# Performance work log

Measured on AMD Instinct MI355X. Metric: run time of the kernel, lower is better.

Reference implementation:

```python
import jax, jax.numpy as jnp
import numpy as np

D = 32        # number of TT cores (d)
R = 16        # tt_rank
B = 262144    # batch size


def setup_inputs() -> dict:
    key = jax.random.key(0)
    k1, k2, k3, k4 = jax.random.split(key, 4)
    return {
        "X": jax.random.randint(k1, (B, D), 0, 2, dtype=jnp.int32),
        "core_first": jax.random.normal(k2, (1, R, 2), dtype=jnp.float32),
        "cores_mid": jax.random.normal(k3, (D - 2, R, R, 2), dtype=jnp.float32),
        "core_last": jax.random.normal(k4, (R, 1, 2), dtype=jnp.float32),
    }


def reference(X, core_first, cores_mid, core_last):
    # First core: cores[0][:, :, X[:,0]] -> [1, R, B] -> permute -> [B, 1, R].
    # We carry the squeezed [B, R] row vector instead of [B, 1, R].
    carry0 = jnp.take(core_first[0], X[:, 0], axis=-1).T  # [B, R]

    def step(carry, inp):
        core, idx = inp                       # core: [R, R, 2], idx: [B]
        c = jnp.take(core, idx, axis=2)       # gathered core: [R, R, B]
        new = jnp.einsum('br,rsb->bs', carry, c)  # batched (1xR)@(RxR)
        return new, None

    # Middle cores i = 1 .. D-2 (sequential chain, data-dependent).
    carry, _ = jax.lax.scan(step, carry0, (cores_mid, X[:, 1:D - 1].T))

    # Last core: cores[-1][:, :, X[:,-1]] -> [R, 1, B]; contract to scalar per batch.
    c_last = jnp.take(core_last[:, 0, :], X[:, -1], axis=-1)  # [R, B]
    out = jnp.einsum('br,rb->b', carry, c_last)               # [B]  (squeeze of [B,1,1])
    return out
```

## Files before the change

kernel.cpp:

```cpp
#include <hip/hip_runtime.h>


#define R 16
#define TT_D 32
#define BATCH 262144

#define OFF_V4   0
#define OFF_A    256
#define OFF_B    (256 + 1*4096)
#define OFF_C    (256 + 2*4096)
#define OFF_Dm   (256 + 3*4096)
#define OFF_E    (256 + 4*4096)
#define OFF_F    (256 + 5*4096)
#define OFF_W4   (256 + 6*4096)
#define OFF_V8   (OFF_W4 + 256)
#define OFF_P8   (OFF_V8 + 4096)
#define OFF_Q8   (OFF_P8 + 65536)
#define OFF_W8   (OFF_Q8 + 65536)
#define OFF_V16  (OFF_W8 + 4096)
#define OFF_W16  (OFF_V16 + 1048576)
#define WS_FLOATS (OFF_W16 + 1048576)

__global__ __launch_bounds__(256) void tt_nibble(const float* __restrict__ cf,
                                                 const float* __restrict__ cm,
                                                 const float* __restrict__ cl,
                                                 float* __restrict__ ws) {
    const int tbl = blockIdx.x;
    const int t = threadIdx.x;

    if (tbl >= 1 && tbl <= 6) {
        const int e = t >> 4, r = t & 15;
        const int base = 3 + (tbl - 1) * 4;
        const int b0 = (e >> 3) & 1, b1 = (e >> 2) & 1, b2 = (e >> 1) & 1, b3 = e & 1;
        float v[R], nv[R];
        const float* M0 = cm + base * 512;
        #pragma unroll
        for (int s2 = 0; s2 < R; s2++) v[s2] = M0[(r * 16 + s2) * 2 + b0];
        const int bits[3] = { b1, b2, b3 };
        for (int k = 1; k <= 3; k++) {
            const float* M = cm + (base + k) * 512;
            const int bb = bits[k - 1];
            #pragma unroll
            for (int s2 = 0; s2 < R; s2++) {
                float acc = 0.f;
                #pragma unroll
                for (int tt = 0; tt < R; tt++) acc += v[tt] * M[(tt * 16 + s2) * 2 + bb];
                nv[s2] = acc;
            }
            #pragma unroll
            for (int s2 = 0; s2 < R; s2++) v[s2] = nv[s2];
        }
        float* o = ws + OFF_A + (tbl - 1) * 4096 + e * 256 + r * 16;
        #pragma unroll
        for (int s2 = 0; s2 < R; s2++) o[s2] = v[s2];
    } else if (tbl == 0) {
        if (t < 16) {
            const int e = t;
            const int b0 = (e >> 3) & 1, b1 = (e >> 2) & 1, b2 = (e >> 1) & 1, b3 = e & 1;
            float v[R], nv[R];
            #pragma unroll
            for (int s2 = 0; s2 < R; s2++) v[s2] = cf[s2 * 2 + b0];
            const int bits[3] = { b1, b2, b3 };
            for (int k = 1; k <= 3; k++) {
                const float* M = cm + (k - 1) * 512;
                const int bb = bits[k - 1];
                #pragma unroll
                for (int s2 = 0; s2 < R; s2++) {
                    float acc = 0.f;
                    #pragma unroll
                    for (int tt = 0; tt < R; tt++) acc += v[tt] * M[(tt * 16 + s2) * 2 + bb];
                    nv[s2] = acc;
                }
                #pragma unroll
                for (int s2 = 0; s2 < R; s2++) v[s2] = nv[s2];
            }
            float* o = ws + OFF_V4 + e * 16;
            #pragma unroll
            for (int s2 = 0; s2 < R; s2++) o[s2] = v[s2];
        }
    } else {
        if (t < 16) {
            const int e = t;
            const int b0 = (e >> 3) & 1, b1 = (e >> 2) & 1, b2 = (e >> 1) & 1, b3 = e & 1;
            float w[R], nw[R];
            #pragma unroll
            for (int r2 = 0; r2 < R; r2++) w[r2] = cl[r2 * 2 + b3];
            const int cores[3] = { 29, 28, 27 };
            const int bits[3] = { b2, b1, b0 };
            for (int k = 0; k < 3; k++) {
                const float* M = cm + cores[k] * 512;
                const int bb = bits[k];
                #pragma unroll
                for (int r2 = 0; r2 < R; r2++) {
                    float acc = 0.f;
                    #pragma unroll
                    for (int tt = 0; tt < R; tt++) acc += M[(r2 * 16 + tt) * 2 + bb] * w[tt];
                    nw[r2] = acc;
                }
                #pragma unroll
                for (int r2 = 0; r2 < R; r2++) w[r2] = nw[r2];
            }
            float* o = ws + OFF_W4 + e * 16;
            #pragma unroll
            for (int r2 = 0; r2 < R; r2++) o[r2] = w[r2];
        }
    }
}

__global__ __launch_bounds__(256) void tt_byte(float* __restrict__ ws) {
    const int g = blockIdx.x;
    const int t = threadIdx.x;
    if (g < 32) {
        const bool isP = (g < 16);
        const int idx = (isP ? g : g - 16) * 256 + t;
        const int e = idx >> 4, r = idx & 15;
        const int h = e >> 4, l = e & 15;
        const float* Hm = ws + (isP ? OFF_B : OFF_Dm) + h * 256;
        const float* Lm = ws + (isP ? OFF_C : OFF_E) + l * 256;
        float hrow[R];
        #pragma unroll
        for (int k = 0; k < R; k++) hrow[k] = Hm[r * 16 + k];
        float outv[R];
        #pragma unroll
        for (int s2 = 0; s2 < R; s2++) outv[s2] = 0.f;
        #pragma unroll
        for (int k = 0; k < R; k++) {
            const float a = hrow[k];
            #pragma unroll
            for (int s2 = 0; s2 < R; s2++) outv[s2] += a * Lm[k * 16 + s2];
        }
        float* o = ws + (isP ? OFF_P8 : OFF_Q8) + e * 256 + r * 16;
        #pragma unroll
        for (int s2 = 0; s2 < R; s2++) o[s2] = outv[s2];
    } else if (g == 32) {
        const int e = t, h = e >> 4, l = e & 15;
        const float* v4 = ws + OFF_V4 + h * 16;
        const float* Am = ws + OFF_A + l * 256;
        float outv[R];
        #pragma unroll
        for (int s2 = 0; s2 < R; s2++) outv[s2] = 0.f;
        #pragma unroll
        for (int k = 0; k < R; k++) {
            const float a = v4[k];
            #pragma unroll
            for (int s2 = 0; s2 < R; s2++) outv[s2] += a * Am[k * 16 + s2];
        }
        float* o = ws + OFF_V8 + e * 16;
        #pragma unroll
        for (int s2 = 0; s2 < R; s2++) o[s2] = outv[s2];
    } else {
        const int e = t, h = e >> 4, l = e & 15;
        const float* Fm = ws + OFF_F + h * 256;
        const float* w4 = ws + OFF_W4 + l * 16;
        float outv[R];
        #pragma unroll
        for (int r2 = 0; r2 < R; r2++) {
            float acc = 0.f;
            #pragma unroll
            for (int k = 0; k < R; k++) acc += Fm[r2 * 16 + k] * w4[k];
            outv[r2] = acc;
        }
        float* o = ws + OFF_W8 + e * 16;
        #pragma unroll
        for (int r2 = 0; r2 < R; r2++) o[r2] = outv[r2];
    }
}

__global__ __launch_bounds__(256) void tt_final(float* __restrict__ ws) {
    const int t = threadIdx.x;
    if (blockIdx.x < 256) {
        const int h = blockIdx.x, l = t;
        __shared__ float sv[16];
        if (t < 16) sv[t] = ws[OFF_V8 + h * 16 + t];
        __syncthreads();
        const float* P = ws + OFF_P8 + l * 256;
        float outv[R];
        #pragma unroll
        for (int s2 = 0; s2 < R; s2++) outv[s2] = 0.f;
        #pragma unroll
        for (int r2 = 0; r2 < R; r2++) {
            const float a = sv[r2];
            #pragma unroll
            for (int s2 = 0; s2 < R; s2++) outv[s2] += a * P[r2 * 16 + s2];
        }
        float* o = ws + OFF_V16 + (size_t)(h * 256 + l) * 16;
        #pragma unroll
        for (int s2 = 0; s2 < R; s2++) o[s2] = outv[s2];
    } else {
        const int h = blockIdx.x - 256, l = t;
        __shared__ float sQ[256];
        sQ[t] = ws[OFF_Q8 + h * 256 + t];
        __syncthreads();
        const float* wv = ws + OFF_W8 + l * 16;
        float w[R];
        #pragma unroll
        for (int k = 0; k < R; k++) w[k] = wv[k];
        float outv[R];
        #pragma unroll
        for (int r2 = 0; r2 < R; r2++) {
            float acc = 0.f;
            #pragma unroll
            for (int k = 0; k < R; k++) acc += sQ[r2 * 16 + k] * w[k];
            outv[r2] = acc;
        }
        float* o = ws + OFF_W16 + (size_t)(h * 256 + l) * 16;
        #pragma unroll
        for (int r2 = 0; r2 < R; r2++) o[r2] = outv[r2];
    }
}

__global__ __launch_bounds__(256) void tt_main(const int* __restrict__ X,
                                               const float* __restrict__ ws,
                                               float* __restrict__ out) {
    const int b = blockIdx.x * 256 + threadIdx.x;
    const int4* Xr = (const int4*)(X + (size_t)b * TT_D);
    int xv[TT_D];
    #pragma unroll
    for (int q = 0; q < 8; q++) {
        int4 c = Xr[q];
        xv[q * 4 + 0] = c.x; xv[q * 4 + 1] = c.y; xv[q * 4 + 2] = c.z; xv[q * 4 + 3] = c.w;
    }
    unsigned p = 0, s = 0;
    #pragma unroll
    for (int i = 0; i < 16; i++) p = (p << 1) | (unsigned)(xv[i] & 1);
    #pragma unroll
    for (int i = 16; i < 32; i++) s = (s << 1) | (unsigned)(xv[i] & 1);

    const float4* v = (const float4*)(ws + OFF_V16 + (size_t)p * 16);
    const float4* w = (const float4*)(ws + OFF_W16 + (size_t)s * 16);
    float acc = 0.f;
    #pragma unroll
    for (int k = 0; k < 4; k++) {
        float4 a = v[k], c = w[k];
        acc += a.x * c.x + a.y * c.y + a.z * c.z + a.w * c.w;
    }
    out[b] = acc;
}

__global__ __launch_bounds__(256) void tt_direct(const int* __restrict__ X,
                                                 const float* __restrict__ cf,
                                                 const float* __restrict__ cm,
                                                 const float* __restrict__ cl,
                                                 float* __restrict__ out) {
    __shared__ float scm[30 * 16 * 16 * 2];
    for (int i = threadIdx.x; i < 30 * 16 * 16 * 2; i += blockDim.x) scm[i] = cm[i];
    __syncthreads();
    const int b = blockIdx.x * blockDim.x + threadIdx.x;
    if (b >= BATCH) return;
    const int* xr = X + (size_t)b * TT_D;
    float v[R], nv[R];
    const int x0 = xr[0] & 1;
    #pragma unroll
    for (int r = 0; r < R; r++) v[r] = cf[r * 2 + x0];
    for (int i = 1; i <= 30; i++) {
        const int bit = xr[i] & 1;
        const float* M = scm + (i - 1) * 512;
        #pragma unroll
        for (int s2 = 0; s2 < R; s2++) {
            float acc = 0.f;
            #pragma unroll
            for (int r = 0; r < R; r++) acc += v[r] * M[(r * 16 + s2) * 2 + bit];
            nv[s2] = acc;
        }
        #pragma unroll
        for (int s2 = 0; s2 < R; s2++) v[s2] = nv[s2];
    }
    const int xl = xr[31] & 1;
    float acc = 0.f;
    #pragma unroll
    for (int r = 0; r < R; r++) acc += v[r] * cl[r * 2 + xl];
    out[b] = acc;
}

extern "C" void kernel_launch(void* const* d_in, const int* in_sizes, int n_in,
                              void* d_out, int out_size, void* d_ws, size_t ws_size,
                              hipStream_t stream) {
    const int* X = (const int*)d_in[0];
    const float* cf = (const float*)d_in[1];
    const float* cm = (const float*)d_in[2];
    const float* cl = (const float*)d_in[3];
    float* out = (float*)d_out;

    if (ws_size >= (size_t)WS_FLOATS * sizeof(float)) {
        float* ws = (float*)d_ws;
        tt_nibble<<<8, 256, 0, stream>>>(cf, cm, cl, ws);
        tt_byte<<<34, 256, 0, stream>>>(ws);
        tt_final<<<512, 256, 0, stream>>>(ws);
        tt_main<<<BATCH / 256, 256, 0, stream>>>(X, ws, out);
    } else {
        tt_direct<<<(BATCH + 255) / 256, 256, 0, stream>>>(X, cf, cm, cl, out);
    }
}
```

Before: 122.8 us.

## Merge nibble and byte table builds into one kernel; process two rows per thread

Folds the nibble-level and byte-level table construction into one kernel that stages the cores in shared memory with a transposed layout, which cuts one launch and the global round trip for the intermediate tables. The main lookup kernel now handles two batch rows per thread, using nontemporal vector loads of X and a packed float2 nontemporal store. This reduces launch overhead and aims for better memory-level parallelism, at the cost of higher register use and less parallelism inside the build kernel.

```diff
diff --git a/kernel.cpp b/kernel.cpp
--- a/kernel.cpp
+++ b/kernel.cpp
@@ -5,15 +5,7 @@
 #define TT_D 32
 #define BATCH 262144
 
-#define OFF_V4   0
-#define OFF_A    256
-#define OFF_B    (256 + 1*4096)
-#define OFF_C    (256 + 2*4096)
-#define OFF_Dm   (256 + 3*4096)
-#define OFF_E    (256 + 4*4096)
-#define OFF_F    (256 + 5*4096)
-#define OFF_W4   (256 + 6*4096)
-#define OFF_V8   (OFF_W4 + 256)
+#define OFF_V8   0
 #define OFF_P8   (OFF_V8 + 4096)
 #define OFF_Q8   (OFF_P8 + 65536)
 #define OFF_W8   (OFF_Q8 + 65536)
@@ -21,220 +13,272 @@
 #define OFF_W16  (OFF_V16 + 1048576)
 #define WS_FLOATS (OFF_W16 + 1048576)
 
-__global__ __launch_bounds__(256) void tt_nibble(const float* __restrict__ cf,
+typedef int   v4i __attribute__((ext_vector_type(4)));
+typedef float v4f __attribute__((ext_vector_type(4)));
+typedef float v2f __attribute__((ext_vector_type(2)));
+
+__device__ inline void row_chain4(const float* __restrict__ Lc, int cbase, int e, int r,
+                                  float* __restrict__ v) {
+    const int b0 = (e >> 3) & 1, b1 = (e >> 2) & 1, b2 = (e >> 1) & 1, b3 = e & 1;
+    #pragma unroll
+    for (int s = 0; s < 16; s++) v[s] = Lc[((((cbase * 2 + b0) * 16) + s) << 4) + r];
+    const int bits[3] = { b1, b2, b3 };
+    #pragma unroll
+    for (int k = 1; k <= 3; k++) {
+        const float* M = Lc + (((cbase + k) * 2 + bits[k - 1]) << 8);
+        float nv[16];
+        #pragma unroll
+        for (int s2 = 0; s2 < 16; s2++) {
+            float acc = 0.f;
+            #pragma unroll
+            for (int r2 = 0; r2 < 16; r2++) acc += v[r2] * M[(s2 << 4) + r2];
+            nv[s2] = acc;
+        }
+        #pragma unroll
+        for (int s2 = 0; s2 < 16; s2++) v[s2] = nv[s2];
+    }
+}
+
+__global__ __launch_bounds__(256) void tt_build1(const float* __restrict__ cf,
                                                  const float* __restrict__ cm,
                                                  const float* __restrict__ cl,
                                                  float* __restrict__ ws) {
-    const int tbl = blockIdx.x;
+    __shared__ float sh[12288];
+    const int g = blockIdx.x;
     const int t = threadIdx.x;
 
-    if (tbl >= 1 && tbl <= 6) {
-        const int e = t >> 4, r = t & 15;
-        const int base = 3 + (tbl - 1) * 4;
-        const int b0 = (e >> 3) & 1, b1 = (e >> 2) & 1, b2 = (e >> 1) & 1, b3 = e & 1;
-        float v[R], nv[R];
-        const float* M0 = cm + base * 512;
-        #pragma unroll
-        for (int s2 = 0; s2 < R; s2++) v[s2] = M0[(r * 16 + s2) * 2 + b0];
-        const int bits[3] = { b1, b2, b3 };
-        for (int k = 1; k <= 3; k++) {
-            const float* M = cm + (base + k) * 512;
-            const int bb = bits[k - 1];
-            #pragma unroll
-            for (int s2 = 0; s2 < R; s2++) {
-                float acc = 0.f;
-                #pragma unroll
-                for (int tt = 0; tt < R; tt++) acc += v[tt] * M[(tt * 16 + s2) * 2 + bb];
-                nv[s2] = acc;
-            }
-            #pragma unroll
-            for (int s2 = 0; s2 < R; s2++) v[s2] = nv[s2];
-        }
-        float* o = ws + OFF_A + (tbl - 1) * 4096 + e * 256 + r * 16;
-        #pragma unroll
-        for (int s2 = 0; s2 < R; s2++) o[s2] = v[s2];
-    } else if (tbl == 0) {
+    if (g < 32) {
+        const bool isP = (g < 16);
+        const int gb = isP ? g : g - 16;
+        const int coreBase = isP ? 7 : 15;
+        for (int i = t; i < 8 * 512; i += 256) {
+            const int c = i >> 9, j = i & 511;
+            const int x = j & 1, s = (j >> 1) & 15, r = j >> 5;
+            sh[(((c * 2 + x) * 16) + s) * 16 + r] = cm[coreBase * 512 + i];
+        }
+        __syncthreads();
+        {
+            const int e = t >> 4, r = t & 15;
+            float v[16];
+            row_chain4(sh, 4, e, r, v);
+            #pragma unroll
+            for (int s = 0; s < 16; s++) sh[8192 + (e << 8) + (r << 4) + s] = v[s];
+        }
+        if (t < 16) {
+            float v[16];
+            row_chain4(sh, 0, gb, t, v);
+            #pragma unroll
+            for (int s = 0; s < 16; s++) sh[4096 + (t << 4) + s] = v[s];
+        }
+        __syncthreads();
+        {
+            const int l = t >> 4, r = t & 15;
+            float h[16], outv[16];
+            #pragma unroll
+            for (int k = 0; k < 16; k++) h[k] = sh[4096 + (r << 4) + k];
+            #pragma unroll
+            for (int s2 = 0; s2 < 16; s2++) outv[s2] = 0.f;
+            #pragma unroll
+            for (int k = 0; k < 16; k++) {
+                const float a = h[k];
+                #pragma unroll
+                for (int s2 = 0; s2 < 16; s2++) outv[s2] += a * sh[8192 + (l << 8) + (k << 4) + s2];
+            }
+            const int e8 = gb * 16 + l;
+            float* o = ws + (isP ? OFF_P8 : OFF_Q8) + (e8 << 8) + (r << 4);
+            #pragma unroll
+            for (int s2 = 0; s2 < 16; s2++) o[s2] = outv[s2];
+        }
+    } else if (g == 32) {
+        for (int i = t; i < 7 * 512; i += 256) {
+            const int c = i >> 9, j = i & 511;
+            const int x = j & 1, s = (j >> 1) & 15, r = j >> 5;
+            sh[(((c * 2 + x) * 16) + s) * 16 + r] = cm[i];
+        }
+        if (t < 32) sh[8192 + t] = cf[t];
+        __syncthreads();
+        {
+            const int e = t >> 4, r = t & 15;
+            float v[16];
+            row_chain4(sh, 3, e, r, v);
+            #pragma unroll
+            for (int s = 0; s < 16; s++) sh[4096 + (e << 8) + (r << 4) + s] = v[s];
+        }
         if (t < 16) {
             const int e = t;
             const int b0 = (e >> 3) & 1, b1 = (e >> 2) & 1, b2 = (e >> 1) & 1, b3 = e & 1;
-            float v[R], nv[R];
-            #pragma unroll
-            for (int s2 = 0; s2 < R; s2++) v[s2] = cf[s2 * 2 + b0];
+            float v[16];
+            #pragma unroll
+            for (int s = 0; s < 16; s++) v[s] = sh[8192 + s * 2 + b0];
             const int bits[3] = { b1, b2, b3 };
+            #pragma unroll
             for (int k = 1; k <= 3; k++) {
-                const float* M = cm + (k - 1) * 512;
-                const int bb = bits[k - 1];
-                #pragma unroll
-                for (int s2 = 0; s2 < R; s2++) {
+                const float* M = sh + (((k - 1) * 2 + bits[k - 1]) << 8);
+                float nv[16];
+                #pragma unroll
+                for (int s2 = 0; s2 < 16; s2++) {
                     float acc = 0.f;
                     #pragma unroll
-                    for (int tt = 0; tt < R; tt++) acc += v[tt] * M[(tt * 16 + s2) * 2 + bb];
+                    for (int r2 = 0; r2 < 16; r2++) acc += v[r2] * M[(s2 << 4) + r2];
                     nv[s2] = acc;
                 }
                 #pragma unroll
-                for (int s2 = 0; s2 < R; s2++) v[s2] = nv[s2];
-            }
-            float* o = ws + OFF_V4 + e * 16;
-            #pragma unroll
-            for (int s2 = 0; s2 < R; s2++) o[s2] = v[s2];
+                for (int s2 = 0; s2 < 16; s2++) v[s2] = nv[s2];
+            }
+            #pragma unroll
+            for (int s = 0; s < 16; s++) sh[8256 + (e << 4) + s] = v[s];
+        }
+        __syncthreads();
+        {
+            const int h = t >> 4, l = t & 15;
+            float outv[16];
+            #pragma unroll
+            for (int s2 = 0; s2 < 16; s2++) outv[s2] = 0.f;
+            #pragma unroll
+            for (int k = 0; k < 16; k++) {
+                const float a = sh[8256 + (h << 4) + k];
+                #pragma unroll
+                for (int s2 = 0; s2 < 16; s2++) outv[s2] += a * sh[4096 + (l << 8) + (k << 4) + s2];
+            }
+            float* o = ws + OFF_V8 + (t << 4);
+            #pragma unroll
+            for (int s2 = 0; s2 < 16; s2++) o[s2] = outv[s2];
         }
     } else {
+        for (int i = t; i < 7 * 512; i += 256) {
+            const int c = i >> 9, j = i & 511;
+            const int x = j & 1, s = (j >> 1) & 15, r = j >> 5;
+            sh[(((c * 2 + x) * 16) + s) * 16 + r] = cm[23 * 512 + i];
+        }
+        if (t < 32) sh[8192 + t] = cl[t];
+        __syncthreads();
+        {
+            const int e = t >> 4, r = t & 15;
+            float v[16];
+            row_chain4(sh, 0, e, r, v);
+            #pragma unroll
+            for (int s = 0; s < 16; s++) sh[4096 + (e << 8) + (r << 4) + s] = v[s];
+        }
         if (t < 16) {
             const int e = t;
             const int b0 = (e >> 3) & 1, b1 = (e >> 2) & 1, b2 = (e >> 1) & 1, b3 = e & 1;
-            float w[R], nw[R];
-            #pragma unroll
-            for (int r2 = 0; r2 < R; r2++) w[r2] = cl[r2 * 2 + b3];
-            const int cores[3] = { 29, 28, 27 };
-            const int bits[3] = { b2, b1, b0 };
+            float w[16];
+            #pragma unroll
+            for (int r2 = 0; r2 < 16; r2++) w[r2] = sh[8192 + r2 * 2 + b3];
+            const int cidx[3] = { 6, 5, 4 };
+            const int bidx[3] = { b2, b1, b0 };
+            #pragma unroll
             for (int k = 0; k < 3; k++) {
-                const float* M = cm + cores[k] * 512;
-                const int bb = bits[k];
-                #pragma unroll
-                for (int r2 = 0; r2 < R; r2++) {
+                const float* M = sh + ((cidx[k] * 2 + bidx[k]) << 8);
+                float nw[16];
+                #pragma unroll
+                for (int r2 = 0; r2 < 16; r2++) {
                     float acc = 0.f;
                     #pragma unroll
-                    for (int tt = 0; tt < R; tt++) acc += M[(r2 * 16 + tt) * 2 + bb] * w[tt];
+                    for (int kk = 0; kk < 16; kk++) acc += M[(kk << 4) + r2] * w[kk];
                     nw[r2] = acc;
                 }
                 #pragma unroll
-                for (int r2 = 0; r2 < R; r2++) w[r2] = nw[r2];
-            }
-            float* o = ws + OFF_W4 + e * 16;
-            #pragma unroll
-            for (int r2 = 0; r2 < R; r2++) o[r2] = w[r2];
-        }
-    }
-}
-
-__global__ __launch_bounds__(256) void tt_byte(float* __restrict__ ws) {
-    const int g = blockIdx.x;
-    const int t = threadIdx.x;
-    if (g < 32) {
-        const bool isP = (g < 16);
-        const int idx = (isP ? g : g - 16) * 256 + t;
-        const int e = idx >> 4, r = idx & 15;
-        const int h = e >> 4, l = e & 15;
-        const float* Hm = ws + (isP ? OFF_B : OFF_Dm) + h * 256;
-        const float* Lm = ws + (isP ? OFF_C : OFF_E) + l * 256;
-        float hrow[R];
-        #pragma unroll
-        for (int k = 0; k < R; k++) hrow[k] = Hm[r * 16 + k];
-        float outv[R];
-        #pragma unroll
-        for (int s2 = 0; s2 < R; s2++) outv[s2] = 0.f;
-        #pragma unroll
-        for (int k = 0; k < R; k++) {
-            const float a = hrow[k];
-            #pragma unroll
-            for (int s2 = 0; s2 < R; s2++) outv[s2] += a * Lm[k * 16 + s2];
-        }
-        float* o = ws + (isP ? OFF_P8 : OFF_Q8) + e * 256 + r * 16;
-        #pragma unroll
-        for (int s2 = 0; s2 < R; s2++) o[s2] = outv[s2];
-    } else if (g == 32) {
-        const int e = t, h = e >> 4, l = e & 15;
-        const float* v4 = ws + OFF_V4 + h * 16;
-        const float* Am = ws + OFF_A + l * 256;
-        float outv[R];
-        #pragma unroll
-        for (int s2 = 0; s2 < R; s2++) outv[s2] = 0.f;
-        #pragma unroll
-        for (int k = 0; k < R; k++) {
-            const float a = v4[k];
-            #pragma unroll
-            for (int s2 = 0; s2 < R; s2++) outv[s2] += a * Am[k * 16 + s2];
-        }
-        float* o = ws + OFF_V8 + e * 16;
-        #pragma unroll
-        for (int s2 = 0; s2 < R; s2++) o[s2] = outv[s2];
-    } else {
-        const int e = t, h = e >> 4, l = e & 15;
-        const float* Fm = ws + OFF_F + h * 256;
-        const float* w4 = ws + OFF_W4 + l * 16;
-        float outv[R];
-        #pragma unroll
-        for (int r2 = 0; r2 < R; r2++) {
-            float acc = 0.f;
-            #pragma unroll
-            for (int k = 0; k < R; k++) acc += Fm[r2 * 16 + k] * w4[k];
-            outv[r2] = acc;
-        }
-        float* o = ws + OFF_W8 + e * 16;
-        #pragma unroll
-        for (int r2 = 0; r2 < R; r2++) o[r2] = outv[r2];
-    }
-}
-
-__global__ __launch_bounds__(256) void tt_final(float* __restrict__ ws) {
+                for (int r2 = 0; r2 < 16; r2++) w[r2] = nw[r2];
+            }
+            #pragma unroll
+            for (int r2 = 0; r2 < 16; r2++) sh[8256 + (e << 4) + r2] = w[r2];
+        }
+        __syncthreads();
+        {
+            const int h = t >> 4, l = t & 15;
+            float w4[16], outv[16];
+            #pragma unroll
+            for (int k = 0; k < 16; k++) w4[k] = sh[8256 + (l << 4) + k];
+            #pragma unroll
+            for (int r2 = 0; r2 < 16; r2++) {
+                float acc = 0.f;
+                #pragma unroll
+                for (int k = 0; k < 16; k++) acc += sh[4096 + (h << 8) + (r2 << 4) + k] * w4[k];
+                outv[r2] = acc;
+            }
+            float* o = ws + OFF_W8 + (t << 4);
+            #pragma unroll
+            for (int r2 = 0; r2 < 16; r2++) o[r2] = outv[r2];
+        }
+    }
+}
+
+__global__ __launch_bounds__(256) void tt_build2(float* __restrict__ ws) {
     const int t = threadIdx.x;
     if (blockIdx.x < 256) {
         const int h = blockIdx.x, l = t;
         __shared__ float sv[16];
         if (t < 16) sv[t] = ws[OFF_V8 + h * 16 + t];
         __syncthreads();
-        const float* P = ws + OFF_P8 + l * 256;
-        float outv[R];
-        #pragma unroll
-        for (int s2 = 0; s2 < R; s2++) outv[s2] = 0.f;
-        #pragma unroll
-        for (int r2 = 0; r2 < R; r2++) {
+        const float* P = ws + OFF_P8 + (l << 8);
+        float outv[16];
+        #pragma unroll
+        for (int s2 = 0; s2 < 16; s2++) outv[s2] = 0.f;
+        #pragma unroll
+        for (int r2 = 0; r2 < 16; r2++) {
             const float a = sv[r2];
             #pragma unroll
-            for (int s2 = 0; s2 < R; s2++) outv[s2] += a * P[r2 * 16 + s2];
-        }
-        float* o = ws + OFF_V16 + (size_t)(h * 256 + l) * 16;
-        #pragma unroll
-        for (int s2 = 0; s2 < R; s2++) o[s2] = outv[s2];
+            for (int s2 = 0; s2 < 16; s2++) outv[s2] += a * P[(r2 << 4) + s2];
+        }
+        float* o = ws + OFF_V16 + (size_t)((h << 8) + l) * 16;
+        #pragma unroll
+        for (int s2 = 0; s2 < 16; s2++) o[s2] = outv[s2];
     } else {
         const int h = blockIdx.x - 256, l = t;
         __shared__ float sQ[256];
-        sQ[t] = ws[OFF_Q8 + h * 256 + t];
-        __syncthreads();
-        const float* wv = ws + OFF_W8 + l * 16;
-        float w[R];
-        #pragma unroll
-        for (int k = 0; k < R; k++) w[k] = wv[k];
-        float outv[R];
-        #pragma unroll
-        for (int r2 = 0; r2 < R; r2++) {
+        sQ[t] = ws[OFF_Q8 + (h << 8) + t];
+        __syncthreads();
+        const float* wv = ws + OFF_W8 + (l << 4);
+        float w[16];
+        #pragma unroll
+        for (int k = 0; k < 16; k++) w[k] = wv[k];
+        float outv[16];
+        #pragma unroll
+        for (int r2 = 0; r2 < 16; r2++) {
             float acc = 0.f;
             #pragma unroll
-            for (int k = 0; k < R; k++) acc += sQ[r2 * 16 + k] * w[k];
+            for (int k = 0; k < 16; k++) acc += sQ[(r2 << 4) + k] * w[k];
             outv[r2] = acc;
         }
-        float* o = ws + OFF_W16 + (size_t)(h * 256 + l) * 16;
-        #pragma unroll
-        for (int r2 = 0; r2 < R; r2++) o[r2] = outv[r2];
-    }
-}
-
-__global__ __launch_bounds__(256) void tt_main(const int* __restrict__ X,
-                                               const float* __restrict__ ws,
-                                               float* __restrict__ out) {
-    const int b = blockIdx.x * 256 + threadIdx.x;
-    const int4* Xr = (const int4*)(X + (size_t)b * TT_D);
-    int xv[TT_D];
-    #pragma unroll
-    for (int q = 0; q < 8; q++) {
-        int4 c = Xr[q];
-        xv[q * 4 + 0] = c.x; xv[q * 4 + 1] = c.y; xv[q * 4 + 2] = c.z; xv[q * 4 + 3] = c.w;
-    }
-    unsigned p = 0, s = 0;
-    #pragma unroll
-    for (int i = 0; i < 16; i++) p = (p << 1) | (unsigned)(xv[i] & 1);
-    #pragma unroll
-    for (int i = 16; i < 32; i++) s = (s << 1) | (unsigned)(xv[i] & 1);
-
-    const float4* v = (const float4*)(ws + OFF_V16 + (size_t)p * 16);
-    const float4* w = (const float4*)(ws + OFF_W16 + (size_t)s * 16);
-    float acc = 0.f;
-    #pragma unroll
-    for (int k = 0; k < 4; k++) {
-        float4 a = v[k], c = w[k];
-        acc += a.x * c.x + a.y * c.y + a.z * c.z + a.w * c.w;
-    }
-    out[b] = acc;
+        float* o = ws + OFF_W16 + (size_t)((h << 8) + l) * 16;
+        #pragma unroll
+        for (int r2 = 0; r2 < 16; r2++) o[r2] = outv[r2];
+    }
+}
+
+__global__ __launch_bounds__(256) void tt_main2(const int* __restrict__ X,
+                                                const float* __restrict__ ws,
+                                                float* __restrict__ out) {
+    const int tid = blockIdx.x * 256 + threadIdx.x;
+    const v4i* Xr = (const v4i*)(X + (size_t)tid * 64);
+    v4i c[16];
+    #pragma unroll
+    for (int q = 0; q < 16; q++) c[q] = __builtin_nontemporal_load(Xr + q);
+
+    unsigned key[4] = { 0u, 0u, 0u, 0u };
+    #pragma unroll
+    for (int q = 0; q < 16; q++) {
+        const unsigned nib = ((unsigned)(c[q].x & 1) << 3) | ((unsigned)(c[q].y & 1) << 2) |
+                             ((unsigned)(c[q].z & 1) << 1) | (unsigned)(c[q].w & 1);
+        key[q >> 2] = (key[q >> 2] << 4) | nib;
+    }
+
+    const v4f* v0 = (const v4f*)(ws + OFF_V16 + (size_t)key[0] * 16);
+    const v4f* w0 = (const v4f*)(ws + OFF_W16 + (size_t)key[1] * 16);
+    const v4f* v1 = (const v4f*)(ws + OFF_V16 + (size_t)key[2] * 16);
+    const v4f* w1 = (const v4f*)(ws + OFF_W16 + (size_t)key[3] * 16);
+
+    v4f acc0 = { 0.f, 0.f, 0.f, 0.f }, acc1 = { 0.f, 0.f, 0.f, 0.f };
+    #pragma unroll
+    for (int k = 0; k < 4; k++) acc0 += v0[k] * w0[k];
+    #pragma unroll
+    for (int k = 0; k < 4; k++) acc1 += v1[k] * w1[k];
+
+    v2f res;
+    res.x = acc0.x + acc0.y + acc0.z + acc0.w;
+    res.y = acc1.x + acc1.y + acc1.z + acc1.w;
+    __builtin_nontemporal_store(res, (v2f*)(out + (size_t)tid * 2));
 }
 
 __global__ __launch_bounds__(256) void tt_direct(const int* __restrict__ X,
@@ -283,10 +327,9 @@
 
     if (ws_size >= (size_t)WS_FLOATS * sizeof(float)) {
         float* ws = (float*)d_ws;
-        tt_nibble<<<8, 256, 0, stream>>>(cf, cm, cl, ws);
-        tt_byte<<<34, 256, 0, stream>>>(ws);
-        tt_final<<<512, 256, 0, stream>>>(ws);
-        tt_main<<<BATCH / 256, 256, 0, stream>>>(X, ws, out);
+        tt_build1<<<34, 256, 0, stream>>>(cf, cm, cl, ws);
+        tt_build2<<<512, 256, 0, stream>>>(ws);
+        tt_main2<<<BATCH / 512, 256, 0, stream>>>(X, ws, out);
     } else {
         tt_direct<<<(BATCH + 255) / 256, 256, 0, stream>>>(X, cf, cm, cl, out);
     }
```

Result: slower. 135.1 us (+10.0%).
